# Kernel tuning notes

Measured on AMD Instinct MI355X. Metric: run time of the kernel, lower is better.

## Reference

```python
import jax, jax.numpy as jnp
import numpy as np

K = 5000  # module's self.dim

def setup_inputs() -> dict:
    key = jax.random.key(0)
    x = jax.random.normal(key, (50_000_000,), dtype=jnp.float32)
    return {"x": x}

def reference(x):
    # top-k values and their indices (lax.top_k returns them sorted by value,
    # but the subsequent argsort over indices restores original-index order,
    # matching torch.topk(sorted=False) + argsort + gather exactly)
    vals, idx = jax.lax.top_k(x, K)          # [K], [K]
    order = jnp.argsort(idx)                 # permutation restoring input order
    return vals[order]                       # [K] order-preserving top-k subset
```

## Files before the change

### kernel.cpp

```cpp
#include <hip/hip_runtime.h>

#define K_TOP 5000
#define NBIN 2048
#define CAND_LDS 1024
#define NB_BUCKET 4096
#define CAND_STAGE 12288
#define TARGET_SAMPLED 94u

__device__ __forceinline__ unsigned f2key(float f) {
    unsigned u = __float_as_uint(f);
    return (u & 0x80000000u) ? ~u : (u | 0x80000000u);
}
__device__ __forceinline__ float key2f(unsigned k) {
    unsigned u = (k & 0x80000000u) ? (k ^ 0x80000000u) : ~k;
    return __uint_as_float(u);
}

__global__ __launch_bounds__(256) void k_sample(const float4* __restrict__ x4, long n4,
                                                unsigned* __restrict__ hist,
                                                unsigned* __restrict__ ctrl) {
    __shared__ unsigned lh[NBIN];
    __shared__ unsigned gs[64];
    __shared__ unsigned lastFlag;
    for (int i = threadIdx.x; i < NBIN; i += 256) lh[i] = 0;
    __syncthreads();
    int wave = threadIdx.x >> 6;
    int lane = threadIdx.x & 63;
    long gw = (long)blockIdx.x * 4 + wave;
    long totW = (long)gridDim.x * 4;
    long nChunk = (n4 + 8191) / 8192;
    for (long c = gw; c < nChunk; c += totW) {
        long i = c * 8192 + lane;
        if (i < n4) {
            float4 v = x4[i];
            atomicAdd(&lh[f2key(v.x) >> 21], 1u);
            atomicAdd(&lh[f2key(v.y) >> 21], 1u);
            atomicAdd(&lh[f2key(v.z) >> 21], 1u);
            atomicAdd(&lh[f2key(v.w) >> 21], 1u);
        }
    }
    __syncthreads();
    for (int i = threadIdx.x; i < NBIN; i += 256) {
        unsigned c = lh[i];
        if (c) atomicAdd(&hist[i], c);
    }
    __threadfence();
    if (threadIdx.x == 0)
        lastFlag = (atomicAdd(&ctrl[4], 1u) == gridDim.x - 1) ? 1u : 0u;
    __syncthreads();
    if (!lastFlag) return;
    __threadfence();
    for (int i = threadIdx.x; i < NBIN; i += 256)
        lh[i] = __hip_atomic_load(&hist[i], __ATOMIC_RELAXED, __HIP_MEMORY_SCOPE_AGENT);
    __syncthreads();
    int t = threadIdx.x;
    if (t < 64) {
        unsigned s = 0;
        for (int j = 0; j < 32; j++) s += lh[t * 32 + j];
        gs[t] = s;
    }
    __syncthreads();
    if (t == 0) {
        unsigned cum = 0;
        int g = 63;
        for (; g > 0; g--) { if (cum + gs[g] >= TARGET_SAMPLED) break; cum += gs[g]; }
        int b = g * 32 + 31;
        for (; b > g * 32; b--) { if (cum + lh[b] >= TARGET_SAMPLED) break; cum += lh[b]; }
        ctrl[1] = ((unsigned)b) << 21;
    }
}

__global__ __launch_bounds__(256) void k_compact(const float4* __restrict__ x4, long n4,
                                                 long n, const float* __restrict__ x,
                                                 unsigned* __restrict__ ctrl,
                                                 unsigned* __restrict__ candKey,
                                                 unsigned* __restrict__ candIdx,
                                                 unsigned capC) {
    __shared__ unsigned sKey[CAND_LDS], sIdx[CAND_LDS];
    __shared__ unsigned sCnt, sBase;
    if (threadIdx.x == 0) sCnt = 0;
    __syncthreads();
    unsigned L = ctrl[1];
    unsigned* candCount = &ctrl[0];

    int tail = (int)(n & 3);
    if (blockIdx.x == 0 && threadIdx.x < tail) {
        unsigned k = f2key(x[n4 * 4 + threadIdx.x]);
        if (k >= L) {
            unsigned p = atomicAdd(&sCnt, 1u);
            if (p < CAND_LDS) { sKey[p] = k; sIdx[p] = (unsigned)(n4 * 4 + threadIdx.x); }
            else {
                unsigned q = atomicAdd(candCount, 1u);
                if (q < capC) { candKey[q] = k; candIdx[q] = (unsigned)(n4 * 4 + threadIdx.x); }
            }
        }
    }

#define PROC(vv, inb, ii)                                                            \
        if (inb) {                                                                   \
            unsigned kk, bb = (unsigned)((ii) * 4);                                  \
            kk = f2key((vv).x);                                                      \
            if (kk >= L) { unsigned p = atomicAdd(&sCnt, 1u);                        \
                if (p < CAND_LDS) { sKey[p] = kk; sIdx[p] = bb; }                    \
                else { unsigned q = atomicAdd(candCount, 1u);                        \
                       if (q < capC) { candKey[q] = kk; candIdx[q] = bb; } } }       \
            kk = f2key((vv).y);                                                      \
            if (kk >= L) { unsigned p = atomicAdd(&sCnt, 1u);                        \
                if (p < CAND_LDS) { sKey[p] = kk; sIdx[p] = bb + 1; }                \
                else { unsigned q = atomicAdd(candCount, 1u);                        \
                       if (q < capC) { candKey[q] = kk; candIdx[q] = bb + 1; } } }   \
            kk = f2key((vv).z);                                                      \
            if (kk >= L) { unsigned p = atomicAdd(&sCnt, 1u);                        \
                if (p < CAND_LDS) { sKey[p] = kk; sIdx[p] = bb + 2; }                \
                else { unsigned q = atomicAdd(candCount, 1u);                        \
                       if (q < capC) { candKey[q] = kk; candIdx[q] = bb + 2; } } }   \
            kk = f2key((vv).w);                                                      \
            if (kk >= L) { unsigned p = atomicAdd(&sCnt, 1u);                        \
                if (p < CAND_LDS) { sKey[p] = kk; sIdx[p] = bb + 3; }                \
                else { unsigned q = atomicAdd(candCount, 1u);                        \
                       if (q < capC) { candKey[q] = kk; candIdx[q] = bb + 3; } } }   \
        }

    long tiles = (n4 + 2047) >> 11;
    for (long tile = blockIdx.x; tile < tiles; tile += gridDim.x) {
        long base = tile << 11;
        long i0 = base + threadIdx.x;
        float4 v[8];
        long  ii[8];
        bool  in[8];
        #pragma unroll
        for (int j = 0; j < 8; j++) {
            ii[j] = i0 + (long)j * 256;
            in[j] = ii[j] < n4;
            if (in[j]) v[j] = x4[ii[j]];
        }
        #pragma unroll
        for (int j = 0; j < 8; j++) {
            PROC(v[j], in[j], ii[j])
        }
    }
#undef PROC
    __syncthreads();
    unsigned cnt = sCnt; if (cnt > CAND_LDS) cnt = CAND_LDS;
    if (threadIdx.x == 0) sBase = atomicAdd(candCount, cnt);
    __syncthreads();
    unsigned bp = sBase;
    for (unsigned i = threadIdx.x; i < cnt; i += 256) {
        unsigned q = bp + i;
        if (q < capC) { candKey[q] = sKey[i]; candIdx[q] = sIdx[i]; }
    }
}

__global__ __launch_bounds__(1024) void k_final(const unsigned* __restrict__ candKey,
                                                const unsigned* __restrict__ candIdx,
                                                unsigned* __restrict__ ctrl, unsigned capC,
                                                unsigned* __restrict__ selKey,
                                                unsigned* __restrict__ selIdx,
                                                unsigned* __restrict__ selKeyS,
                                                unsigned* __restrict__ selIdxS,
                                                float* __restrict__ out, long n, int bshift) {
    __shared__ unsigned cK[CAND_STAGE];
    __shared__ unsigned h[NB_BUCKET * 2];
    __shared__ unsigned selL[K_TOP];
    __shared__ unsigned selIL[K_TOP];
    __shared__ unsigned part[1024];
    __shared__ unsigned part2[32];
    __shared__ unsigned res[2];
    __shared__ unsigned sScalar;
    const int t = threadIdx.x;
    const int lane = t & 63;
    unsigned Nc = ctrl[0]; if (Nc > capC) Nc = capC;
    unsigned L = ctrl[1];
    unsigned ns = (Nc < CAND_STAGE) ? Nc : CAND_STAGE;

    for (unsigned i = t; i < ns; i += 1024) cK[i] = candKey[i];
    __syncthreads();

    unsigned mk = 0;
    for (unsigned i = t; i < ns; i += 1024) { unsigned k = cK[i]; if (k > mk) mk = k; }
    for (unsigned i = ns + t; i < Nc; i += 1024) { unsigned k = candKey[i]; if (k > mk) mk = k; }
    part[t] = mk;
    __syncthreads();
    if (t < 32) { unsigned m = 0; for (int j = 0; j < 32; j++) { unsigned v = part[t * 32 + j]; if (v > m) m = v; } part2[t] = m; }
    __syncthreads();
    if (t == 0) { unsigned m = 0; for (int j = 0; j < 32; j++) if (part2[j] > m) m = part2[j]; sScalar = m; }
    __syncthreads();
    unsigned maxK = sScalar;

    unsigned lo = L, target = K_TOP;
    unsigned range = maxK - lo;
    int shift = 0;
    while ((range >> shift) >= NBIN) shift++;
    for (;;) {
        int nb = (int)(range >> shift) + 1;
        for (int i = t; i < nb; i += 1024) h[i] = 0;
        __syncthreads();
        for (unsigned i = t; i < ns; i += 1024) {
            unsigned d = cK[i] - lo;
            if (d <= range) atomicAdd(&h[d >> shift], 1u);
        }
        for (unsigned i = ns + t; i < Nc; i += 1024) {
            unsigned d = candKey[i] - lo;
            if (d <= range) atomicAdd(&h[d >> shift], 1u);
        }
        __syncthreads();
        int ng = (nb + 31) >> 5;
        if (t < ng) {
            unsigned s = 0; int b0 = t * 32, e = b0 + 32; if (e > nb) e = nb;
            for (int j = b0; j < e; j++) s += h[j];
            part[t] = s;
        }
        __syncthreads();
        if (t == 0) {
            unsigned cum = 0; int g = ng - 1;
            for (; g > 0; g--) { if (cum + part[g] >= target) break; cum += part[g]; }
            int hi2 = g * 32 + 31; if (hi2 > nb - 1) hi2 = nb - 1;
            int b = hi2;
            for (; b > g * 32; b--) { if (cum + h[b] >= target) break; cum += h[b]; }
            res[0] = (unsigned)b; res[1] = target - cum;
        }
        __syncthreads();
        lo += res[0] << shift; target = res[1];
        if (shift == 0) break;
        range = (1u << shift) - 1;
        shift = (shift > 11) ? shift - 11 : 0;
    }
    unsigned T = lo, R = target;

    {
        unsigned loc = 0;
        for (unsigned i = t; i < ns; i += 1024) loc += (cK[i] == T) ? 1u : 0u;
        for (unsigned i = ns + t; i < Nc; i += 1024) loc += (candKey[i] == T) ? 1u : 0u;
        part[t] = loc;
        __syncthreads();
        if (t < 32) { unsigned s = 0; for (int j = 0; j < 32; j++) s += part[t * 32 + j]; part2[t] = s; }
        __syncthreads();
        if (t == 0) { unsigned s = 0; for (int j = 0; j < 32; j++) s += part2[j]; sScalar = s; }
        __syncthreads();
    }
    unsigned cntEq = sScalar;
    unsigned idxCut = 0xFFFFFFFFu;
    if (cntEq != R) {
        unsigned lo2 = 0, tgt = R;
        unsigned range2 = (unsigned)(n - 1);
        int sh = 0;
        while ((range2 >> sh) >= NBIN) sh++;
        for (;;) {
            int nb = (int)(range2 >> sh) + 1;
            for (int i = t; i < nb; i += 1024) h[i] = 0;
            __syncthreads();
            for (unsigned i = t; i < ns; i += 1024)
                if (cK[i] == T) {
                    unsigned d = candIdx[i] - lo2;
                    if (d <= range2) atomicAdd(&h[d >> sh], 1u);
                }
            for (unsigned i = ns + t; i < Nc; i += 1024)
                if (candKey[i] == T) {
                    unsigned d = candIdx[i] - lo2;
                    if (d <= range2) atomicAdd(&h[d >> sh], 1u);
                }
            __syncthreads();
            int ng = (nb + 31) >> 5;
            if (t < ng) {
                unsigned s = 0; int b0 = t * 32, e = b0 + 32; if (e > nb) e = nb;
                for (int j = b0; j < e; j++) s += h[j];
                part[t] = s;
            }
            __syncthreads();
            if (t == 0) {
                unsigned cum = 0; int g = 0;
                for (; g < ng - 1; g++) { if (cum + part[g] >= tgt) break; cum += part[g]; }
                int b = g * 32; int hi2 = g * 32 + 31; if (hi2 > nb - 1) hi2 = nb - 1;
                for (; b < hi2; b++) { if (cum + h[b] >= tgt) break; cum += h[b]; }
                res[0] = (unsigned)b; res[1] = tgt - cum;
            }
            __syncthreads();
            lo2 += res[0] << sh; tgt = res[1];
            if (sh == 0) break;
            range2 = (1u << sh) - 1;
            sh = (sh > 11) ? sh - 11 : 0;
        }
        idxCut = lo2;
    }
    __syncthreads();

    for (int i = t; i < NB_BUCKET; i += 1024) h[i] = 0;
    if (t == 0) sScalar = 0;
    __syncthreads();
    for (unsigned i = t; i < Nc; i += 1024) {
        unsigned k = (i < ns) ? cK[i] : candKey[i];
        unsigned id = candIdx[i];
        bool sel = (k > T) || (k == T && id <= idxCut);
        unsigned long long m = __ballot(sel);
        if (m) {
            int leader = (int)__ffsll((unsigned long long)m) - 1;
            unsigned base = 0;
            if (lane == leader) base = atomicAdd(&sScalar, (unsigned)__popcll(m));
            base = __shfl(base, leader);
            if (sel) {
                unsigned p = base + (unsigned)__popcll(m & ((1ull << lane) - 1ull));
                if (p < K_TOP) {
                    selL[p] = k; selIL[p] = id;
                    atomicAdd(&h[id >> bshift], 1u);
                }
            }
        }
    }
    __syncthreads();
    unsigned nSel = sScalar; if (nSel > K_TOP) nSel = K_TOP;

    unsigned* bc = h;
    unsigned* bs = h + NB_BUCKET;
    { unsigned s = 0; for (int j = 0; j < 4; j++) s += bc[t * 4 + j]; part[t] = s; }
    __syncthreads();
    if (t < 32) { unsigned s = 0; for (int j = 0; j < 32; j++) s += part[t * 32 + j]; part2[t] = s; }
    __syncthreads();
    if (t == 0) { unsigned run = 0; for (int j = 0; j < 32; j++) { unsigned v = part2[j]; part2[j] = run; run += v; } }
    __syncthreads();
    if (t < 32) { unsigned run = part2[t]; for (int j = 0; j < 32; j++) { int id2 = t * 32 + j; unsigned v = part[id2]; part[id2] = run; run += v; } }
    __syncthreads();
    { unsigned run = part[t]; for (int j = 0; j < 4; j++) { bs[t * 4 + j] = run; run += bc[t * 4 + j]; } }
    __syncthreads();

    unsigned* sKeyS = cK;
    unsigned* sIdxS = cK + K_TOP;
    for (unsigned g = t; g < nSel; g += 1024) {
        unsigned id = selIL[g];
        unsigned b = id >> bshift;
        unsigned p = atomicAdd(&bs[b], 1u);
        if (p < K_TOP) { sKeyS[p] = selL[g]; sIdxS[p] = id; }
    }
    __syncthreads();

    for (int j = 0; j < 4; j++) {
        int b = t * 4 + j;
        unsigned cnt = bc[b];
        if (!cnt) continue;
        unsigned s = bs[b] - cnt;
        for (unsigned i = 0; i < cnt; i++) {
            unsigned mi = i, mv = sIdxS[s + i];
            for (unsigned q = i + 1; q < cnt; q++) {
                unsigned v = sIdxS[s + q];
                if (v < mv) { mv = v; mi = q; }
            }
            if (mi != i) {
                unsigned ti = sIdxS[s + i]; sIdxS[s + i] = sIdxS[s + mi]; sIdxS[s + mi] = ti;
                unsigned tk = sKeyS[s + i]; sKeyS[s + i] = sKeyS[s + mi]; sKeyS[s + mi] = tk;
            }
            out[s + i] = key2f(sKeyS[s + i]);
        }
    }
}

extern "C" void kernel_launch(void* const* d_in, const int* in_sizes, int n_in,
                              void* d_out, int out_size, void* d_ws, size_t ws_size,
                              hipStream_t stream) {
    const float* x = (const float*)d_in[0];
    long n = in_sizes[0];
    float* out = (float*)d_out;
    unsigned* w = (unsigned*)d_ws;

    unsigned* hist    = w;
    unsigned* ctrl    = w + 2048;
    unsigned* selKey  = w + 2056;
    unsigned* selIdx  = w + 7056;
    unsigned* selKeyS = w + 12056;
    unsigned* selIdxS = w + 17056;
    const size_t CAND_BASE = 24576;
    size_t words = ws_size / 4;
    unsigned capC = 0;
    if (words > CAND_BASE + 64) {
        size_t c = (words - CAND_BASE) / 2;
        if (c > (size_t)(4u << 20)) c = (size_t)(4u << 20);
        capC = (unsigned)c;
    }
    unsigned* candKey = w + CAND_BASE;
    unsigned* candIdx = candKey + capC;

    int bshift = 0;
    while (((n - 1) >> bshift) >= NB_BUCKET) bshift++;

    hipMemsetAsync(d_ws, 0, 2056u * 4u + 32u, stream);

    long n4 = n / 4;
    k_sample<<<256, 256, 0, stream>>>((const float4*)x, n4, hist, ctrl);
    k_compact<<<2048, 256, 0, stream>>>((const float4*)x, n4, n, x, ctrl,
                                        candKey, candIdx, capC);
    k_final<<<1, 1024, 0, stream>>>(candKey, candIdx, ctrl, capC,
                                    selKey, selIdx, selKeyS, selIdxS, out, n, bshift);
}
```

Measured before the change: 349.3 us.

## Fuse compaction and final selection into one kernel via last-block completion

Merges the candidate compaction kernel and the single-block final selection kernel into one 1024-thread kernel. Each block processes four virtual 256-thread tiles, flushes its LDS candidates, then the last block to finish, found with an atomic counter, runs the final top-k selection and ordering. This removes a kernel launch and the gap between launches. In exchange the compaction blocks carry the large LDS footprint of the final stage, which lowers occupancy during the bandwidth-bound scan, and candidate reads switch to agent-scope atomic loads.

Result: slower. 475.7 us (+36.2%).

```diff
diff --git a/kernel.cpp b/kernel.cpp
--- a/kernel.cpp
+++ b/kernel.cpp
@@ -14,6 +14,9 @@
 __device__ __forceinline__ float key2f(unsigned k) {
     unsigned u = (k & 0x80000000u) ? (k ^ 0x80000000u) : ~k;
     return __uint_as_float(u);
+}
+__device__ __forceinline__ unsigned agld(const unsigned* p) {
+    return __hip_atomic_load(p, __ATOMIC_RELAXED, __HIP_MEMORY_SCOPE_AGENT);
 }
 
 __global__ __launch_bounds__(256) void k_sample(const float4* __restrict__ x4, long n4,
@@ -51,7 +54,7 @@
     if (!lastFlag) return;
     __threadfence();
     for (int i = threadIdx.x; i < NBIN; i += 256)
-        lh[i] = __hip_atomic_load(&hist[i], __ATOMIC_RELAXED, __HIP_MEMORY_SCOPE_AGENT);
+        lh[i] = agld(&hist[i]);
     __syncthreads();
     int t = threadIdx.x;
     if (t < 64) {
@@ -70,14 +73,25 @@
     }
 }
 
-__global__ __launch_bounds__(256) void k_compact(const float4* __restrict__ x4, long n4,
-                                                 long n, const float* __restrict__ x,
-                                                 unsigned* __restrict__ ctrl,
-                                                 unsigned* __restrict__ candKey,
-                                                 unsigned* __restrict__ candIdx,
-                                                 unsigned capC) {
-    __shared__ unsigned sKey[CAND_LDS], sIdx[CAND_LDS];
-    __shared__ unsigned sCnt, sBase;
+__global__ __launch_bounds__(1024) void k_fused(const float4* __restrict__ x4, long n4,
+                                                long n, const float* __restrict__ x,
+                                                unsigned* __restrict__ ctrl,
+                                                unsigned* __restrict__ candKey,
+                                                unsigned* __restrict__ candIdx,
+                                                unsigned capC,
+                                                float* __restrict__ out, int bshift) {
+    __shared__ unsigned cK[CAND_STAGE];
+    __shared__ unsigned h[NB_BUCKET * 2];
+    __shared__ unsigned selL[K_TOP];
+    __shared__ unsigned selIL[K_TOP];
+    __shared__ unsigned part[1024];
+    __shared__ unsigned part2[32];
+    __shared__ unsigned res[2];
+    __shared__ unsigned sScalar;
+    __shared__ unsigned sCnt, sBase, lastFlag;
+
+    unsigned* sKey = selL;
+    unsigned* sIdx = selIL;
     if (threadIdx.x == 0) sCnt = 0;
     __syncthreads();
     unsigned L = ctrl[1];
@@ -121,64 +135,59 @@
                        if (q < capC) { candKey[q] = kk; candIdx[q] = bb + 3; } } }   \
         }
 
-    long tiles = (n4 + 2047) >> 11;
-    for (long tile = blockIdx.x; tile < tiles; tile += gridDim.x) {
-        long base = tile << 11;
-        long i0 = base + threadIdx.x;
-        float4 v[8];
-        long  ii[8];
-        bool  in[8];
-        #pragma unroll
-        for (int j = 0; j < 8; j++) {
-            ii[j] = i0 + (long)j * 256;
-            in[j] = ii[j] < n4;
-            if (in[j]) v[j] = x4[ii[j]];
-        }
-        #pragma unroll
-        for (int j = 0; j < 8; j++) {
-            PROC(v[j], in[j], ii[j])
+    {
+        long vblk = (long)blockIdx.x * 4 + (threadIdx.x >> 8);
+        int lane256 = threadIdx.x & 255;
+        long tiles = (n4 + 2047) >> 11;
+        for (long tile = vblk; tile < tiles; tile += 2048) {
+            long base = tile << 11;
+            long i0 = base + lane256;
+            float4 v[8];
+            long  ii[8];
+            bool  in[8];
+            #pragma unroll
+            for (int j = 0; j < 8; j++) {
+                ii[j] = i0 + (long)j * 256;
+                in[j] = ii[j] < n4;
+                if (in[j]) v[j] = x4[ii[j]];
+            }
+            #pragma unroll
+            for (int j = 0; j < 8; j++) {
+                PROC(v[j], in[j], ii[j])
+            }
         }
     }
 #undef PROC
     __syncthreads();
-    unsigned cnt = sCnt; if (cnt > CAND_LDS) cnt = CAND_LDS;
-    if (threadIdx.x == 0) sBase = atomicAdd(candCount, cnt);
-    __syncthreads();
-    unsigned bp = sBase;
-    for (unsigned i = threadIdx.x; i < cnt; i += 256) {
-        unsigned q = bp + i;
-        if (q < capC) { candKey[q] = sKey[i]; candIdx[q] = sIdx[i]; }
-    }
-}
-
-__global__ __launch_bounds__(1024) void k_final(const unsigned* __restrict__ candKey,
-                                                const unsigned* __restrict__ candIdx,
-                                                unsigned* __restrict__ ctrl, unsigned capC,
-                                                unsigned* __restrict__ selKey,
-                                                unsigned* __restrict__ selIdx,
-                                                unsigned* __restrict__ selKeyS,
-                                                unsigned* __restrict__ selIdxS,
-                                                float* __restrict__ out, long n, int bshift) {
-    __shared__ unsigned cK[CAND_STAGE];
-    __shared__ unsigned h[NB_BUCKET * 2];
-    __shared__ unsigned selL[K_TOP];
-    __shared__ unsigned selIL[K_TOP];
-    __shared__ unsigned part[1024];
-    __shared__ unsigned part2[32];
-    __shared__ unsigned res[2];
-    __shared__ unsigned sScalar;
+    {
+        unsigned cnt = sCnt; if (cnt > CAND_LDS) cnt = CAND_LDS;
+        if (threadIdx.x == 0) sBase = atomicAdd(candCount, cnt);
+        __syncthreads();
+        unsigned bp = sBase;
+        for (unsigned i = threadIdx.x; i < cnt; i += 1024) {
+            unsigned q = bp + i;
+            if (q < capC) { candKey[q] = sKey[i]; candIdx[q] = sIdx[i]; }
+        }
+    }
+
+    __threadfence();
+    if (threadIdx.x == 0)
+        lastFlag = (atomicAdd(&ctrl[5], 1u) == gridDim.x - 1) ? 1u : 0u;
+    __syncthreads();
+    if (!lastFlag) return;
+    __threadfence();
+
     const int t = threadIdx.x;
     const int lane = t & 63;
-    unsigned Nc = ctrl[0]; if (Nc > capC) Nc = capC;
-    unsigned L = ctrl[1];
+    unsigned Nc = agld(&ctrl[0]); if (Nc > capC) Nc = capC;
     unsigned ns = (Nc < CAND_STAGE) ? Nc : CAND_STAGE;
 
-    for (unsigned i = t; i < ns; i += 1024) cK[i] = candKey[i];
+    for (unsigned i = t; i < ns; i += 1024) cK[i] = agld(&candKey[i]);
     __syncthreads();
 
     unsigned mk = 0;
     for (unsigned i = t; i < ns; i += 1024) { unsigned k = cK[i]; if (k > mk) mk = k; }
-    for (unsigned i = ns + t; i < Nc; i += 1024) { unsigned k = candKey[i]; if (k > mk) mk = k; }
+    for (unsigned i = ns + t; i < Nc; i += 1024) { unsigned k = agld(&candKey[i]); if (k > mk) mk = k; }
     part[t] = mk;
     __syncthreads();
     if (t < 32) { unsigned m = 0; for (int j = 0; j < 32; j++) { unsigned v = part[t * 32 + j]; if (v > m) m = v; } part2[t] = m; }
@@ -200,7 +209,7 @@
             if (d <= range) atomicAdd(&h[d >> shift], 1u);
         }
         for (unsigned i = ns + t; i < Nc; i += 1024) {
-            unsigned d = candKey[i] - lo;
+            unsigned d = agld(&candKey[i]) - lo;
             if (d <= range) atomicAdd(&h[d >> shift], 1u);
         }
         __syncthreads();
@@ -230,7 +239,7 @@
     {
         unsigned loc = 0;
         for (unsigned i = t; i < ns; i += 1024) loc += (cK[i] == T) ? 1u : 0u;
-        for (unsigned i = ns + t; i < Nc; i += 1024) loc += (candKey[i] == T) ? 1u : 0u;
+        for (unsigned i = ns + t; i < Nc; i += 1024) loc += (agld(&candKey[i]) == T) ? 1u : 0u;
         part[t] = loc;
         __syncthreads();
         if (t < 32) { unsigned s = 0; for (int j = 0; j < 32; j++) s += part[t * 32 + j]; part2[t] = s; }
@@ -251,12 +260,12 @@
             __syncthreads();
             for (unsigned i = t; i < ns; i += 1024)
                 if (cK[i] == T) {
-                    unsigned d = candIdx[i] - lo2;
+                    unsigned d = agld(&candIdx[i]) - lo2;
                     if (d <= range2) atomicAdd(&h[d >> sh], 1u);
                 }
             for (unsigned i = ns + t; i < Nc; i += 1024)
-                if (candKey[i] == T) {
-                    unsigned d = candIdx[i] - lo2;
+                if (agld(&candKey[i]) == T) {
+                    unsigned d = agld(&candIdx[i]) - lo2;
                     if (d <= range2) atomicAdd(&h[d >> sh], 1u);
                 }
             __syncthreads();
@@ -288,8 +297,8 @@
     if (t == 0) sScalar = 0;
     __syncthreads();
     for (unsigned i = t; i < Nc; i += 1024) {
-        unsigned k = (i < ns) ? cK[i] : candKey[i];
-        unsigned id = candIdx[i];
+        unsigned k = (i < ns) ? cK[i] : agld(&candKey[i]);
+        unsigned id = agld(&candIdx[i]);
         bool sel = (k > T) || (k == T && id <= idxCut);
         unsigned long long m = __ballot(sel);
         if (m) {
@@ -362,10 +371,6 @@
 
     unsigned* hist    = w;
     unsigned* ctrl    = w + 2048;
-    unsigned* selKey  = w + 2056;
-    unsigned* selIdx  = w + 7056;
-    unsigned* selKeyS = w + 12056;
-    unsigned* selIdxS = w + 17056;
     const size_t CAND_BASE = 24576;
     size_t words = ws_size / 4;
     unsigned capC = 0;
@@ -384,8 +389,6 @@
 
     long n4 = n / 4;
     k_sample<<<256, 256, 0, stream>>>((const float4*)x, n4, hist, ctrl);
-    k_compact<<<2048, 256, 0, stream>>>((const float4*)x, n4, n, x, ctrl,
-                                        candKey, candIdx, capC);
-    k_final<<<1, 1024, 0, stream>>>(candKey, candIdx, ctrl, capC,
-                                    selKey, selIdx, selKeyS, selIdxS, out, n, bshift);
-}
+    k_fused<<<512, 1024, 0, stream>>>((const float4*)x, n4, n, x, ctrl,
+                                      candKey, candIdx, capC, out, bshift);
+}
```
